# Optimization experiments

Measured on AMD Instinct MI355X. Metric: run time of the kernel, lower is better.

Reference implementation:

```python
import jax, jax.numpy as jnp
import numpy as np


def setup_inputs() -> dict:
    key = jax.random.key(0)
    k1, k2, k3, k4 = jax.random.split(key, 4)
    B, S, D, Y = 8, 2048, 512, 8921
    # xavier_uniform scale for [Y, D] weights
    lim = float(np.sqrt(6.0 / (Y + D)))
    x = jax.random.normal(k1, (B, S, D), dtype=jnp.float32)
    U_w = jax.random.uniform(k2, (Y, D), minval=-lim, maxval=lim, dtype=jnp.float32)
    final_w = jax.random.uniform(k3, (Y, D), minval=-lim, maxval=lim, dtype=jnp.float32)
    final_b = jax.random.normal(k4, (Y,), dtype=jnp.float32) * 0.02
    return {"x": x, "U_w": U_w, "final_w": final_w, "final_b": final_b}


def reference(x, U_w, final_w, final_b):
    # att: [B, Y, S] = U_w @ x^T
    att = jnp.einsum("yd,bsd->bys", U_w, x)
    alpha = jax.nn.softmax(att, axis=2)          # softmax over sequence
    m = jnp.einsum("bys,bsd->byd", alpha, x)      # per-label context [B, Y, D]
    y = jnp.einsum("yd,byd->by", final_w, m) + final_b  # [B, Y]
    return y
```

## Files before the change

kernel.cpp:

```cpp
#include <hip/hip_runtime.h>
#include <hip/hip_bf16.h>

constexpr int B_ = 8;
constexpr int S_ = 2048;
constexpr int D_ = 512;
constexpr int Y_ = 8921;
constexpr int MT_ = 70;

typedef __attribute__((ext_vector_type(8))) __bf16 bf16x8;
typedef __attribute__((ext_vector_type(4))) float f32x4;

__device__ __forceinline__ int swz_el(int row, int ksel8) {
  return row * 64 + ((ksel8 ^ row) & 7) * 8;
}

__global__ __launch_bounds__(256) void cvtW(const float* __restrict__ U,
                                            const float* __restrict__ F,
                                            __hip_bfloat16* __restrict__ wsW) {
  const int c = blockIdx.x * 256 + threadIdx.x;
  const int tile = c >> 11;
  const int row = (c >> 3) & 255;
  const int cs = c & 7;
  const int mt = tile >> 3, kt = tile & 7;
  const int ch = cs ^ (row & 7);
  const int g = row >> 5, h = (row >> 4) & 1, w = row & 15;
  const int y = mt * 128 + g * 16 + w;
  float4 f0 = {0.f, 0.f, 0.f, 0.f}, f1 = {0.f, 0.f, 0.f, 0.f};
  if (y < Y_) {
    const float* src = (h ? F : U) + (size_t)y * D_ + kt * 64 + ch * 8;
    f0 = reinterpret_cast<const float4*>(src)[0];
    f1 = reinterpret_cast<const float4*>(src)[1];
  }
  bf16x8 v;
  v[0] = (__bf16)f0.x; v[1] = (__bf16)f0.y; v[2] = (__bf16)f0.z; v[3] = (__bf16)f0.w;
  v[4] = (__bf16)f1.x; v[5] = (__bf16)f1.y; v[6] = (__bf16)f1.z; v[7] = (__bf16)f1.w;
  *reinterpret_cast<bf16x8*>(wsW + (size_t)c * 8) = v;
}

__global__ __launch_bounds__(256) void cvtX(const float* __restrict__ x,
                                            __hip_bfloat16* __restrict__ wsX) {
  const int c = blockIdx.x * 256 + threadIdx.x;
  const int tile = c >> 11;
  const int row = (c >> 3) & 255;
  const int cs = c & 7;
  const int b = tile >> 6, st = (tile >> 3) & 7, kt = tile & 7;
  const int ch = cs ^ (row & 7);
  const int s = st * 256 + row;
  const float* src = x + ((size_t)b * S_ + s) * D_ + kt * 64 + ch * 8;
  const float4 f0 = reinterpret_cast<const float4*>(src)[0];
  const float4 f1 = reinterpret_cast<const float4*>(src)[1];
  bf16x8 v;
  v[0] = (__bf16)f0.x; v[1] = (__bf16)f0.y; v[2] = (__bf16)f0.z; v[3] = (__bf16)f0.w;
  v[4] = (__bf16)f1.x; v[5] = (__bf16)f1.y; v[6] = (__bf16)f1.z; v[7] = (__bf16)f1.w;
  *reinterpret_cast<bf16x8*>(wsX + (size_t)c * 8) = v;
}

typedef const __attribute__((address_space(1))) void gv_t;
typedef __attribute__((address_space(3))) void lv_t;

__device__ __forceinline__ void gld_lds16(const void* g, void* l) {
  __builtin_amdgcn_global_load_lds((gv_t*)g, (lv_t*)l, 16, 0, 0);
}

__global__ __launch_bounds__(512, 2) void pool_main(
    const __hip_bfloat16* __restrict__ wsW, const __hip_bfloat16* __restrict__ wsX,
    const float* __restrict__ fb, float* __restrict__ out) {
  const int orig = blockIdx.x;
  const int b = orig & 7;
  const int mt = orig >> 3;

  const int tid = threadIdx.x;
  const int lane = tid & 63;
  const int wid = tid >> 6;
  const int wm = wid >> 2;
  const int wn = wid & 3;
  const int l15 = lane & 15;
  const int l4 = lane >> 4;

  extern __shared__ __bf16 lds[];

  const __bf16* Wbase = (const __bf16*)(wsW) + (size_t)mt * 8 * 16384;
  const __bf16* Xbase = (const __bf16*)(wsX) + (size_t)b * 64 * 16384;

  float Lr[4][4];
  float Nr[4][4];
#pragma unroll
  for (int g = 0; g < 4; ++g)
#pragma unroll
    for (int r = 0; r < 4; ++r) { Lr[g][r] = 0.f; Nr[g][r] = 0.f; }

  f32x4 acc[8][4];

  auto stage_tile_all = [&](int t) {
    const int st = t >> 3, kt = t & 7;
    const __bf16* srcA = Wbase + kt * 16384;
    const __bf16* srcX = Xbase + (st * 8 + kt) * 16384;
    __bf16* bufA = &lds[(t & 1) * 32768];
    __bf16* bufX = bufA + 16384;
#pragma unroll
    for (int i = 0; i < 4; ++i) {
      const int cb = wid * 256 + i * 64;
      gld_lds16((const char*)srcA + (size_t)(cb + lane) * 16, (char*)bufA + cb * 16);
    }
#pragma unroll
    for (int i = 0; i < 4; ++i) {
      const int cb = wid * 256 + i * 64;
      gld_lds16((const char*)srcX + (size_t)(cb + lane) * 16, (char*)bufX + cb * 16);
    }
  };

  stage_tile_all(0);
  asm volatile("s_waitcnt vmcnt(0)" ::: "memory");
  __builtin_amdgcn_s_barrier();
  __builtin_amdgcn_sched_barrier(0);

  for (int st = 0; st < 8; ++st) {
#pragma unroll
    for (int m = 0; m < 8; ++m)
#pragma unroll
      for (int n = 0; n < 4; ++n) acc[m][n] = (f32x4){0.f, 0.f, 0.f, 0.f};

    for (int kt = 0; kt < 8; ++kt) {
      const int t = st * 8 + kt;
      const __bf16* A = &lds[(t & 1) * 32768];
      const __bf16* Xl = A + 16384;

      bf16x8 xf[2][4];
#pragma unroll
      for (int p = 0; p < 4; ++p) {
        if (p == 0) {
#pragma unroll
          for (int kk = 0; kk < 2; ++kk)
#pragma unroll
            for (int n = 0; n < 4; ++n)
              xf[kk][n] = *reinterpret_cast<const bf16x8*>(
                  &Xl[swz_el(wn * 64 + n * 16 + l15, kk * 4 + l4)]);
        }
        bf16x8 af[2][2];
#pragma unroll
        for (int j = 0; j < 2; ++j)
#pragma unroll
          for (int kk = 0; kk < 2; ++kk)
            af[j][kk] = *reinterpret_cast<const bf16x8*>(
                &A[swz_el(wm * 128 + (2 * p + j) * 16 + l15, kk * 4 + l4)]);
        if (p == 0 && t + 1 < 64) stage_tile_all(t + 1);

        __builtin_amdgcn_s_barrier();
        __builtin_amdgcn_s_setprio(1);
#pragma unroll
        for (int kk = 0; kk < 2; ++kk)
#pragma unroll
          for (int j = 0; j < 2; ++j)
#pragma unroll
            for (int n = 0; n < 4; ++n)
              acc[2 * p + j][n] = __builtin_amdgcn_mfma_f32_16x16x32_bf16(
                  af[j][kk], xf[kk][n], acc[2 * p + j][n], 0, 0, 0);
        __builtin_amdgcn_s_setprio(0);
        if (p == 3) asm volatile("s_waitcnt vmcnt(0)" ::: "memory");
        __builtin_amdgcn_s_barrier();
      }
      __builtin_amdgcn_sched_barrier(0);
    }

#pragma unroll
    for (int g = 0; g < 4; ++g)
#pragma unroll
      for (int n = 0; n < 4; ++n)
#pragma unroll
        for (int r = 0; r < 4; ++r) {
          const float e = __expf(acc[2 * g][n][r]);
          Lr[g][r] += e;
          Nr[g][r] = fmaf(e, acc[2 * g + 1][n][r], Nr[g][r]);
        }
  }

  __syncthreads();
  float* redL = reinterpret_cast<float*>(lds);
  float* redN = redL + 128;
  if (tid < 256) redL[tid] = 0.f;
  __syncthreads();
#pragma unroll
  for (int g = 0; g < 4; ++g)
#pragma unroll
    for (int r = 0; r < 4; ++r) {
      float l = Lr[g][r], nn = Nr[g][r];
#pragma unroll
      for (int mask = 1; mask <= 8; mask <<= 1) {
        l += __shfl_xor(l, mask);
        nn += __shfl_xor(nn, mask);
      }
      if ((lane & 15) == 0) {
        const int yl = wm * 64 + g * 16 + (l4 << 2) + r;
        atomicAdd(&redL[yl], l);
        atomicAdd(&redN[yl], nn);
      }
    }
  __syncthreads();
  for (int i = tid; i < 128; i += 512) {
    const int y = mt * 128 + i;
    if (y < Y_) out[(size_t)b * Y_ + y] = redN[i] / redL[i] + fb[y];
  }
}

constexpr int FB_BY = 128, FB_BS = 64, FB_BK = 64;

__device__ __forceinline__ int fswz(int row, int k) {
  return row * FB_BK + ((((k >> 3) ^ row) & 7) << 3) + (k & 7);
}

template <int CHUNKS>
__device__ __forceinline__ void fb_stage(const float* __restrict__ gbase, int rstride,
                                         int maxrow, __bf16* lds, int tid) {
#pragma unroll
  for (int i = 0; i < CHUNKS / 256; ++i) {
    const int c = tid + 256 * i;
    const int row = c >> 3;
    const int ch = c & 7;
    float4 f0 = {0.f, 0.f, 0.f, 0.f}, f1 = {0.f, 0.f, 0.f, 0.f};
    if (row < maxrow) {
      const float4* p = reinterpret_cast<const float4*>(gbase + (size_t)row * rstride + ch * 8);
      f0 = p[0]; f1 = p[1];
    }
    bf16x8 v;
    v[0] = (__bf16)f0.x; v[1] = (__bf16)f0.y; v[2] = (__bf16)f0.z; v[3] = (__bf16)f0.w;
    v[4] = (__bf16)f1.x; v[5] = (__bf16)f1.y; v[6] = (__bf16)f1.z; v[7] = (__bf16)f1.w;
    *reinterpret_cast<bf16x8*>(&lds[fswz(row, ch * 8)]) = v;
  }
}

__global__ __launch_bounds__(256) void output_layer_fallback(
    const float* __restrict__ x, const float* __restrict__ Uw,
    const float* __restrict__ Fw, const float* __restrict__ fb,
    float* __restrict__ out) {
  const int b = blockIdx.y;
  const int y0 = blockIdx.x * FB_BY;
  const int tid = threadIdx.x;
  const int lane = tid & 63;
  const int w = tid >> 6;
  const int wm = (w >> 1) * 64, wn = (w & 1) * 32;
  __shared__ __bf16 sU[FB_BY * FB_BK], sF[FB_BY * FB_BK], sX[FB_BS * FB_BK];
  float Ls[4][4], Ns[4][4];
#pragma unroll
  for (int m = 0; m < 4; ++m)
#pragma unroll
    for (int r = 0; r < 4; ++r) { Ls[m][r] = 0.f; Ns[m][r] = 0.f; }
  const float* xb = x + (size_t)b * S_ * D_;
  const int umax = Y_ - y0;
  for (int s0 = 0; s0 < S_; s0 += FB_BS) {
    f32x4 accA[4][2] = {}, accP[4][2] = {};
    for (int k0 = 0; k0 < D_; k0 += FB_BK) {
      __syncthreads();
      fb_stage<FB_BY * 8>(Uw + (size_t)y0 * D_ + k0, D_, umax, sU, tid);
      fb_stage<FB_BY * 8>(Fw + (size_t)y0 * D_ + k0, D_, umax, sF, tid);
      fb_stage<FB_BS * 8>(xb + (size_t)s0 * D_ + k0, D_, FB_BS, sX, tid);
      __syncthreads();
#pragma unroll
      for (int kk = 0; kk < 2; ++kk) {
        const int kb = kk * 32 + (lane >> 4) * 8;
        bf16x8 bx[2];
#pragma unroll
        for (int n = 0; n < 2; ++n)
          bx[n] = *reinterpret_cast<const bf16x8*>(&sX[fswz(wn + n * 16 + (lane & 15), kb)]);
#pragma unroll
        for (int m = 0; m < 4; ++m) {
          const bf16x8 aU = *reinterpret_cast<const bf16x8*>(&sU[fswz(wm + m * 16 + (lane & 15), kb)]);
          const bf16x8 aF = *reinterpret_cast<const bf16x8*>(&sF[fswz(wm + m * 16 + (lane & 15), kb)]);
#pragma unroll
          for (int n = 0; n < 2; ++n) {
            accA[m][n] = __builtin_amdgcn_mfma_f32_16x16x32_bf16(aU, bx[n], accA[m][n], 0, 0, 0);
            accP[m][n] = __builtin_amdgcn_mfma_f32_16x16x32_bf16(aF, bx[n], accP[m][n], 0, 0, 0);
          }
        }
      }
    }
#pragma unroll
    for (int m = 0; m < 4; ++m)
#pragma unroll
      for (int n = 0; n < 2; ++n)
#pragma unroll
        for (int r = 0; r < 4; ++r) {
          const float e = __expf(accA[m][n][r]);
          Ls[m][r] += e;
          Ns[m][r] = fmaf(e, accP[m][n][r], Ns[m][r]);
        }
  }
  __syncthreads();
  float* redL = reinterpret_cast<float*>(sU);
  float* redN = reinterpret_cast<float*>(sF);
  for (int i = tid; i < FB_BY; i += 256) { redL[i] = 0.f; redN[i] = 0.f; }
  __syncthreads();
#pragma unroll
  for (int m = 0; m < 4; ++m)
#pragma unroll
    for (int r = 0; r < 4; ++r) {
      float l = Ls[m][r], nn = Ns[m][r];
#pragma unroll
      for (int mask = 1; mask <= 8; mask <<= 1) {
        l += __shfl_xor(l, mask);
        nn += __shfl_xor(nn, mask);
      }
      if ((lane & 15) == 0) {
        const int yl = wm + m * 16 + ((lane >> 4) << 2) + r;
        atomicAdd(&redL[yl], l);
        atomicAdd(&redN[yl], nn);
      }
    }
  __syncthreads();
  for (int i = tid; i < FB_BY; i += 256) {
    const int y = y0 + i;
    if (y < Y_) out[(size_t)b * Y_ + y] = redN[i] / redL[i] + fb[y];
  }
}

extern "C" void kernel_launch(void* const* d_in, const int* in_sizes, int n_in,
                              void* d_out, int out_size, void* d_ws,
                              size_t ws_size, hipStream_t stream) {
  const float* x = (const float*)d_in[0];
  const float* Uw = (const float*)d_in[1];
  const float* Fw = (const float*)d_in[2];
  const float* fb = (const float*)d_in[3];
  float* out = (float*)d_out;

  constexpr size_t W_EL = (size_t)MT_ * 8 * 16384;
  constexpr size_t X_EL = (size_t)B_ * 64 * 16384;
  constexpr size_t WS_NEED = (W_EL + X_EL) * 2;

  if (ws_size >= WS_NEED) {
    __hip_bfloat16* wsW = (__hip_bfloat16*)d_ws;
    __hip_bfloat16* wsX = wsW + W_EL;

    cvtW<<<dim3((unsigned)(W_EL / 8 / 256)), dim3(256), 0, stream>>>(Uw, Fw, wsW);
    cvtX<<<dim3((unsigned)(X_EL / 8 / 256)), dim3(256), 0, stream>>>(x, wsX);

    hipFuncSetAttribute((const void*)pool_main,
                        hipFuncAttributeMaxDynamicSharedMemorySize, 131072);
    pool_main<<<dim3(MT_ * B_), dim3(512), 131072, stream>>>(wsW, wsX, fb, out);
  } else {
    output_layer_fallback<<<dim3(MT_, B_), dim3(256), 0, stream>>>(x, Uw, Fw, fb, out);
  }
}
```

Baseline: 388.7 us.

## Split sequence across blocks and load X fragments directly into registers

Splits the sequence dimension into 4 groups so the main kernel launches 4x more blocks (2240 instead of 560). Partial softmax sums are accumulated with global atomics, followed by a separate combine kernel that divides and adds the bias. X is stored pre-arranged in MFMA fragment order and read straight from global memory into registers, which shrinks LDS to 64KB of W double-buffering and drops the dynamic shared memory attribute. In exchange it adds extra launches (zeroing and combine), global atomic traffic, and reloads each W tile once per sequence group.

```diff
diff --git a/kernel.cpp b/kernel.cpp
--- a/kernel.cpp
+++ b/kernel.cpp
@@ -6,6 +6,7 @@
 constexpr int D_ = 512;
 constexpr int Y_ = 8921;
 constexpr int MT_ = 70;
+constexpr int SG_ = 4;
 
 typedef __attribute__((ext_vector_type(8))) __bf16 bf16x8;
 typedef __attribute__((ext_vector_type(4))) float f32x4;
@@ -40,13 +41,16 @@
 __global__ __launch_bounds__(256) void cvtX(const float* __restrict__ x,
                                             __hip_bfloat16* __restrict__ wsX) {
   const int c = blockIdx.x * 256 + threadIdx.x;
-  const int tile = c >> 11;
-  const int row = (c >> 3) & 255;
-  const int cs = c & 7;
-  const int b = tile >> 6, st = (tile >> 3) & 7, kt = tile & 7;
-  const int ch = cs ^ (row & 7);
-  const int s = st * 256 + row;
-  const float* src = x + ((size_t)b * S_ + s) * D_ + kt * 64 + ch * 8;
+  const int lane = c & 63;
+  const int idx2 = (c >> 6) & 7;
+  const int wn = (c >> 9) & 3;
+  const int kt = (c >> 11) & 7;
+  const int st = (c >> 14) & 7;
+  const int b = (c >> 17) & 7;
+  const int n = idx2 >> 1, kk = idx2 & 1;
+  const int s = st * 256 + wn * 64 + n * 16 + (lane & 15);
+  const int k = kt * 64 + kk * 32 + (lane >> 4) * 8;
+  const float* src = x + ((size_t)b * S_ + s) * D_ + k;
   const float4 f0 = reinterpret_cast<const float4*>(src)[0];
   const float4 f1 = reinterpret_cast<const float4*>(src)[1];
   bf16x8 v;
@@ -55,6 +59,20 @@
   *reinterpret_cast<bf16x8*>(wsX + (size_t)c * 8) = v;
 }
 
+__global__ __launch_bounds__(256) void zeroLN(float* __restrict__ LN, int n) {
+  const int i = blockIdx.x * 256 + threadIdx.x;
+  if (i < n) LN[i] = 0.f;
+}
+
+__global__ __launch_bounds__(256) void combine(const float* __restrict__ Lg,
+                                               const float* __restrict__ Ng,
+                                               const float* __restrict__ fb,
+                                               float* __restrict__ out) {
+  const int y = blockIdx.x * 256 + threadIdx.x;
+  const int b = blockIdx.y;
+  if (y < Y_) out[(size_t)b * Y_ + y] = Ng[b * Y_ + y] / Lg[b * Y_ + y] + fb[y];
+}
+
 typedef const __attribute__((address_space(1))) void gv_t;
 typedef __attribute__((address_space(3))) void lv_t;
 
@@ -64,10 +82,12 @@
 
 __global__ __launch_bounds__(512, 2) void pool_main(
     const __hip_bfloat16* __restrict__ wsW, const __hip_bfloat16* __restrict__ wsX,
-    const float* __restrict__ fb, float* __restrict__ out) {
-  const int orig = blockIdx.x;
-  const int b = orig & 7;
-  const int mt = orig >> 3;
+    float* __restrict__ Lg, float* __restrict__ Ng) {
+  const int bid = blockIdx.x;
+  const int b = bid & 7;
+  const int r = bid >> 3;
+  const int mt = r % MT_;
+  const int sg = r / MT_;
 
   const int tid = threadIdx.x;
   const int lane = tid & 63;
@@ -77,89 +97,130 @@
   const int l15 = lane & 15;
   const int l4 = lane >> 4;
 
-  extern __shared__ __bf16 lds[];
-
-  const __bf16* Wbase = (const __bf16*)(wsW) + (size_t)mt * 8 * 16384;
-  const __bf16* Xbase = (const __bf16*)(wsX) + (size_t)b * 64 * 16384;
-
-  float Lr[4][4];
-  float Nr[4][4];
+  __shared__ __bf16 lds[2 * 16384];
+
+  const __bf16* Wbase = (const __bf16*)wsW + (size_t)mt * 8 * 16384;
+  const __bf16* Xw = (const __bf16*)wsX + wn * 4096 + lane * 8;
+
+  float Lr[4][4], Nr[4][4];
 #pragma unroll
   for (int g = 0; g < 4; ++g)
 #pragma unroll
-    for (int r = 0; r < 4; ++r) { Lr[g][r] = 0.f; Nr[g][r] = 0.f; }
+    for (int q = 0; q < 4; ++q) { Lr[g][q] = 0.f; Nr[g][q] = 0.f; }
 
   f32x4 acc[8][4];
 
-  auto stage_tile_all = [&](int t) {
-    const int st = t >> 3, kt = t & 7;
-    const __bf16* srcA = Wbase + kt * 16384;
-    const __bf16* srcX = Xbase + (st * 8 + kt) * 16384;
-    __bf16* bufA = &lds[(t & 1) * 32768];
-    __bf16* bufX = bufA + 16384;
+  auto stageA = [&](int ktn, int par) {
+    const __bf16* src = Wbase + ktn * 16384;
+    char* dst = (char*)lds + par * 32768;
 #pragma unroll
     for (int i = 0; i < 4; ++i) {
       const int cb = wid * 256 + i * 64;
-      gld_lds16((const char*)srcA + (size_t)(cb + lane) * 16, (char*)bufA + cb * 16);
-    }
-#pragma unroll
-    for (int i = 0; i < 4; ++i) {
-      const int cb = wid * 256 + i * 64;
-      gld_lds16((const char*)srcX + (size_t)(cb + lane) * 16, (char*)bufX + cb * 16);
+      gld_lds16((const char*)src + (size_t)(cb + lane) * 16, dst + cb * 16);
     }
   };
 
-  stage_tile_all(0);
+  auto xfrag = [&](int st, int kt, int n, int kk) -> bf16x8 {
+    const size_t tile = (size_t)((b * 8 + st) * 8 + kt);
+    return *reinterpret_cast<const bf16x8*>(Xw + tile * 16384 + (n * 2 + kk) * 512);
+  };
+
+  bf16x8 X0[4], X1[4];
+
+  stageA(0, 0);
+#pragma unroll
+  for (int n = 0; n < 4; ++n) X0[n] = xfrag(sg * 2, 0, n, 0);
   asm volatile("s_waitcnt vmcnt(0)" ::: "memory");
   __builtin_amdgcn_s_barrier();
   __builtin_amdgcn_sched_barrier(0);
 
-  for (int st = 0; st < 8; ++st) {
+  for (int si = 0; si < 2; ++si) {
+    const int st = sg * 2 + si;
 #pragma unroll
     for (int m = 0; m < 8; ++m)
 #pragma unroll
       for (int n = 0; n < 4; ++n) acc[m][n] = (f32x4){0.f, 0.f, 0.f, 0.f};
 
+#pragma unroll
     for (int kt = 0; kt < 8; ++kt) {
-      const int t = st * 8 + kt;
-      const __bf16* A = &lds[(t & 1) * 32768];
-      const __bf16* Xl = A + 16384;
-
-      bf16x8 xf[2][4];
-#pragma unroll
-      for (int p = 0; p < 4; ++p) {
-        if (p == 0) {
-#pragma unroll
-          for (int kk = 0; kk < 2; ++kk)
-#pragma unroll
-            for (int n = 0; n < 4; ++n)
-              xf[kk][n] = *reinterpret_cast<const bf16x8*>(
-                  &Xl[swz_el(wn * 64 + n * 16 + l15, kk * 4 + l4)]);
+      const __bf16* A = lds + ((kt & 1) << 14);
+      const bool has_next = !(si == 1 && kt == 7);
+      const int ktn = (kt + 1) & 7;
+      const int stn = sg * 2 + si + (kt == 7 ? 1 : 0);
+
+      {
+        bf16x8 af[4];
+#pragma unroll
+        for (int j = 0; j < 4; ++j)
+          af[j] = *reinterpret_cast<const bf16x8*>(
+              &A[swz_el(wm * 128 + j * 16 + l15, l4)]);
+#pragma unroll
+        for (int n = 0; n < 4; ++n) X1[n] = xfrag(st, kt, n, 1);
+        if (has_next) stageA(ktn, (kt + 1) & 1);
+        __builtin_amdgcn_s_barrier();
+        __builtin_amdgcn_s_setprio(1);
+#pragma unroll
+        for (int j = 0; j < 4; ++j)
+#pragma unroll
+          for (int n = 0; n < 4; ++n)
+            acc[j][n] = __builtin_amdgcn_mfma_f32_16x16x32_bf16(af[j], X0[n], acc[j][n], 0, 0, 0);
+        __builtin_amdgcn_s_setprio(0);
+        __builtin_amdgcn_s_barrier();
+      }
+      {
+        bf16x8 af[4];
+#pragma unroll
+        for (int j = 0; j < 4; ++j)
+          af[j] = *reinterpret_cast<const bf16x8*>(
+              &A[swz_el(wm * 128 + (4 + j) * 16 + l15, l4)]);
+        __builtin_amdgcn_s_barrier();
+        __builtin_amdgcn_s_setprio(1);
+#pragma unroll
+        for (int j = 0; j < 4; ++j)
+#pragma unroll
+          for (int n = 0; n < 4; ++n)
+            acc[4 + j][n] = __builtin_amdgcn_mfma_f32_16x16x32_bf16(af[j], X0[n], acc[4 + j][n], 0, 0, 0);
+        __builtin_amdgcn_s_setprio(0);
+        __builtin_amdgcn_s_barrier();
+      }
+      {
+        bf16x8 af[4];
+#pragma unroll
+        for (int j = 0; j < 4; ++j)
+          af[j] = *reinterpret_cast<const bf16x8*>(
+              &A[swz_el(wm * 128 + j * 16 + l15, 4 + l4)]);
+        if (has_next) {
+#pragma unroll
+          for (int n = 0; n < 4; ++n) X0[n] = xfrag(stn, ktn, n, 0);
         }
-        bf16x8 af[2][2];
-#pragma unroll
-        for (int j = 0; j < 2; ++j)
-#pragma unroll
-          for (int kk = 0; kk < 2; ++kk)
-            af[j][kk] = *reinterpret_cast<const bf16x8*>(
-                &A[swz_el(wm * 128 + (2 * p + j) * 16 + l15, kk * 4 + l4)]);
-        if (p == 0 && t + 1 < 64) stage_tile_all(t + 1);
-
         __builtin_amdgcn_s_barrier();
         __builtin_amdgcn_s_setprio(1);
 #pragma unroll
-        for (int kk = 0; kk < 2; ++kk)
-#pragma unroll
-          for (int j = 0; j < 2; ++j)
-#pragma unroll
-            for (int n = 0; n < 4; ++n)
-              acc[2 * p + j][n] = __builtin_amdgcn_mfma_f32_16x16x32_bf16(
-                  af[j][kk], xf[kk][n], acc[2 * p + j][n], 0, 0, 0);
+        for (int j = 0; j < 4; ++j)
+#pragma unroll
+          for (int n = 0; n < 4; ++n)
+            acc[j][n] = __builtin_amdgcn_mfma_f32_16x16x32_bf16(af[j], X1[n], acc[j][n], 0, 0, 0);
         __builtin_amdgcn_s_setprio(0);
-        if (p == 3) asm volatile("s_waitcnt vmcnt(0)" ::: "memory");
-        __builtin_amdgcn_s_barrier();
-      }
-      __builtin_amdgcn_sched_barrier(0);
+        __builtin_amdgcn_s_barrier();
+      }
+      {
+        bf16x8 af[4];
+#pragma unroll
+        for (int j = 0; j < 4; ++j)
+          af[j] = *reinterpret_cast<const bf16x8*>(
+              &A[swz_el(wm * 128 + (4 + j) * 16 + l15, 4 + l4)]);
+        __builtin_amdgcn_s_barrier();
+        __builtin_amdgcn_s_setprio(1);
+#pragma unroll
+        for (int j = 0; j < 4; ++j)
+#pragma unroll
+          for (int n = 0; n < 4; ++n)
+            acc[4 + j][n] = __builtin_amdgcn_mfma_f32_16x16x32_bf16(af[j], X1[n], acc[4 + j][n], 0, 0, 0);
+        __builtin_amdgcn_s_setprio(0);
+        asm volatile("s_waitcnt vmcnt(0)" ::: "memory");
+        __builtin_amdgcn_s_barrier();
+        __builtin_amdgcn_sched_barrier(0);
+      }
     }
 
 #pragma unroll
@@ -167,10 +228,10 @@
 #pragma unroll
       for (int n = 0; n < 4; ++n)
 #pragma unroll
-        for (int r = 0; r < 4; ++r) {
-          const float e = __expf(acc[2 * g][n][r]);
-          Lr[g][r] += e;
-          Nr[g][r] = fmaf(e, acc[2 * g + 1][n][r], Nr[g][r]);
+        for (int q = 0; q < 4; ++q) {
+          const float e = __expf(acc[2 * g][n][q]);
+          Lr[g][q] += e;
+          Nr[g][q] = fmaf(e, acc[2 * g + 1][n][q], Nr[g][q]);
         }
   }
 
@@ -182,15 +243,15 @@
 #pragma unroll
   for (int g = 0; g < 4; ++g)
 #pragma unroll
-    for (int r = 0; r < 4; ++r) {
-      float l = Lr[g][r], nn = Nr[g][r];
+    for (int q = 0; q < 4; ++q) {
+      float l = Lr[g][q], nn = Nr[g][q];
 #pragma unroll
       for (int mask = 1; mask <= 8; mask <<= 1) {
         l += __shfl_xor(l, mask);
         nn += __shfl_xor(nn, mask);
       }
       if ((lane & 15) == 0) {
-        const int yl = wm * 64 + g * 16 + (l4 << 2) + r;
+        const int yl = wm * 64 + g * 16 + (l4 << 2) + q;
         atomicAdd(&redL[yl], l);
         atomicAdd(&redN[yl], nn);
       }
@@ -198,7 +259,10 @@
   __syncthreads();
   for (int i = tid; i < 128; i += 512) {
     const int y = mt * 128 + i;
-    if (y < Y_) out[(size_t)b * Y_ + y] = redN[i] / redL[i] + fb[y];
+    if (y < Y_) {
+      atomicAdd(&Lg[(size_t)b * Y_ + y], redL[i]);
+      atomicAdd(&Ng[(size_t)b * Y_ + y], redN[i]);
+    }
   }
 }
 
@@ -243,7 +307,7 @@
 #pragma unroll
   for (int m = 0; m < 4; ++m)
 #pragma unroll
-    for (int r = 0; r < 4; ++r) { Ls[m][r] = 0.f; Ns[m][r] = 0.f; }
+    for (int q = 0; q < 4; ++q) { Ls[m][q] = 0.f; Ns[m][q] = 0.f; }
   const float* xb = x + (size_t)b * S_ * D_;
   const int umax = Y_ - y0;
   for (int s0 = 0; s0 < S_; s0 += FB_BS) {
@@ -278,10 +342,10 @@
 #pragma unroll
       for (int n = 0; n < 2; ++n)
 #pragma unroll
-        for (int r = 0; r < 4; ++r) {
-          const float e = __expf(accA[m][n][r]);
-          Ls[m][r] += e;
-          Ns[m][r] = fmaf(e, accP[m][n][r], Ns[m][r]);
+        for (int q = 0; q < 4; ++q) {
+          const float e = __expf(accA[m][n][q]);
+          Ls[m][q] += e;
+          Ns[m][q] = fmaf(e, accP[m][n][q], Ns[m][q]);
         }
   }
   __syncthreads();
@@ -292,15 +356,15 @@
 #pragma unroll
   for (int m = 0; m < 4; ++m)
 #pragma unroll
-    for (int r = 0; r < 4; ++r) {
-      float l = Ls[m][r], nn = Ns[m][r];
+    for (int q = 0; q < 4; ++q) {
+      float l = Ls[m][q], nn = Ns[m][q];
 #pragma unroll
       for (int mask = 1; mask <= 8; mask <<= 1) {
         l += __shfl_xor(l, mask);
         nn += __shfl_xor(nn, mask);
       }
       if ((lane & 15) == 0) {
-        const int yl = wm + m * 16 + ((lane >> 4) << 2) + r;
+        const int yl = wm + m * 16 + ((lane >> 4) << 2) + q;
         atomicAdd(&redL[yl], l);
         atomicAdd(&redN[yl], nn);
       }
@@ -323,18 +387,20 @@
 
   constexpr size_t W_EL = (size_t)MT_ * 8 * 16384;
   constexpr size_t X_EL = (size_t)B_ * 64 * 16384;
-  constexpr size_t WS_NEED = (W_EL + X_EL) * 2;
+  constexpr size_t LN_FL = (size_t)2 * B_ * Y_;
+  constexpr size_t WS_NEED = (W_EL + X_EL) * 2 + LN_FL * 4;
 
   if (ws_size >= WS_NEED) {
     __hip_bfloat16* wsW = (__hip_bfloat16*)d_ws;
     __hip_bfloat16* wsX = wsW + W_EL;
+    float* Lg = (float*)(wsX + X_EL);
+    float* Ng = Lg + (size_t)B_ * Y_;
 
     cvtW<<<dim3((unsigned)(W_EL / 8 / 256)), dim3(256), 0, stream>>>(Uw, Fw, wsW);
     cvtX<<<dim3((unsigned)(X_EL / 8 / 256)), dim3(256), 0, stream>>>(x, wsX);
-
-    hipFuncSetAttribute((const void*)pool_main,
-                        hipFuncAttributeMaxDynamicSharedMemorySize, 131072);
-    pool_main<<<dim3(MT_ * B_), dim3(512), 131072, stream>>>(wsW, wsX, fb, out);
+    zeroLN<<<dim3((unsigned)((LN_FL + 255) / 256)), dim3(256), 0, stream>>>(Lg, (int)LN_FL);
+    pool_main<<<dim3(MT_ * B_ * SG_), dim3(512), 0, stream>>>(wsW, wsX, Lg, Ng);
+    combine<<<dim3((Y_ + 255) / 256, B_), dim3(256), 0, stream>>>(Lg, Ng, fb, out);
   } else {
     output_layer_fallback<<<dim3(MT_, B_), dim3(256), 0, stream>>>(x, Uw, Fw, fb, out);
   }
```

New measurement: 572.3 us. 47.2% more time.
